# Optimization experiments

Hardware: AMD Instinct MI355X
Metric: run time of the kernel (lower is better)

The kernel has to match this reference:

```python
import jax, jax.numpy as jnp
import numpy as np

N_HEAD = 16

def setup_inputs() -> dict:
    key = jax.random.key(0)
    ks = jax.random.split(key, 5)
    B, T, C = 2, 2048, 1024
    s = 1.0 / np.sqrt(C)
    return {
        "x":  jax.random.normal(ks[0], (B, T, C), jnp.float32),
        "Wk": jax.random.normal(ks[1], (C, C), jnp.float32) * s,
        "Wq": jax.random.normal(ks[2], (C, C), jnp.float32) * s,
        "Wv": jax.random.normal(ks[3], (C, C), jnp.float32) * s,
        "Wp": jax.random.normal(ks[4], (C, C), jnp.float32) * s,
    }

def reference(x, Wk, Wq, Wv, Wp):
    B, T, C = x.shape
    H = N_HEAD
    D = C // H
    # torch Linear (bias=False): y = x @ W.T
    def proj(W):
        return (x @ W.T).reshape(B, T, H, D).transpose(0, 2, 1, 3)  # [B,H,T,D]
    q, k, v = proj(Wq), proj(Wk), proj(Wv)
    att = jnp.einsum("bhtd,bhsd->bhts", q, k) / jnp.sqrt(jnp.float32(D))
    causal = jnp.tril(jnp.ones((T, T), dtype=bool))
    att = jnp.where(causal[None, None], att, -jnp.inf)
    att = jax.nn.softmax(att, axis=-1)
    y = jnp.einsum("bhts,bhsd->bhtd", att, v)
    y = y.transpose(0, 2, 1, 3).reshape(B, T, C)
    return y @ Wp.T
```

## Files before the change

### kernel.cpp

```cpp
#include <hip/hip_runtime.h>

typedef unsigned short u16;
typedef unsigned int u32;
typedef unsigned long long u64;
typedef __attribute__((ext_vector_type(8))) short bf16x8;
typedef __attribute__((ext_vector_type(4))) float f32x4;

#define GLOAD16(gp, lp) __builtin_amdgcn_global_load_lds( \
  (const __attribute__((address_space(1))) unsigned int*)(gp), \
  (__attribute__((address_space(3))) unsigned int*)(lp), 16, 0, 0)

__device__ __forceinline__ u16 f2bf(float f) {
  unsigned int u = __builtin_bit_cast(unsigned int, f);
  u += 0x7fffu + ((u >> 16) & 1u);
  return (u16)(u >> 16);
}

__device__ __forceinline__ u32 pk2(float a, float b) {
  return (u32)f2bf(a) | ((u32)f2bf(b) << 16);
}

__global__ __launch_bounds__(256) void cvt_f32_bf16(
    const float* __restrict__ in, u16* __restrict__ out, int n) {
  int i = (blockIdx.x * 256 + threadIdx.x) * 4;
  if (i < n) {
    float4 f = *reinterpret_cast<const float4*>(in + i);
    u64 v = (u64)pk2(f.x, f.y) | ((u64)pk2(f.z, f.w) << 32);
    *reinterpret_cast<u64*>(out + i) = v;
  }
}

__global__ __launch_bounds__(256) void cvt_w4(
    const float* __restrict__ w0, const float* __restrict__ w1,
    const float* __restrict__ w2, const float* __restrict__ w3,
    u16* __restrict__ o0, u16* __restrict__ o1,
    u16* __restrict__ o2, u16* __restrict__ o3) {
  int z = blockIdx.y;
  const float* in = (z == 0) ? w0 : (z == 1) ? w1 : (z == 2) ? w2 : w3;
  u16* out = (z == 0) ? o0 : (z == 1) ? o1 : (z == 2) ? o2 : o3;
  int i = (blockIdx.x * 256 + threadIdx.x) * 4;
  float4 f = *reinterpret_cast<const float4*>(in + i);
  u64 v = (u64)pk2(f.x, f.y) | ((u64)pk2(f.z, f.w) << 32);
  *reinterpret_cast<u64*>(out + i) = v;
}

template<int MODE>
__device__ __forceinline__ void gemm_bt_body(
    const u16* __restrict__ A, const u16* __restrict__ Bw, void* __restrict__ Cout,
    int m0, int n0, float scale) {
  const int K = 1024;
  __shared__ __align__(16) u16 As[2][128 * 32];
  __shared__ __align__(16) u16 Bs[2][128 * 32];
  const int tid = threadIdx.x;
  const int lane = tid & 63, wid = tid >> 6;
  const int wr = wid >> 1, wc = wid & 1;
  const int g = lane >> 4, c = lane & 15;
  f32x4 acc[4][4] = {};

  auto stage = [&](int buf, int k0) {
#pragma unroll
    for (int i = 0; i < 2; ++i) {
      int idx = tid + i * 256;
      int row = idx >> 2, slot = idx & 3;
      int ss = slot ^ (row & 3);
      GLOAD16(A + (size_t)(m0 + row) * K + k0 + ss * 8, &As[buf][idx * 8]);
    }
#pragma unroll
    for (int i = 0; i < 2; ++i) {
      int idx = tid + i * 256;
      int row = idx >> 2, slot = idx & 3;
      int ss = slot ^ (row & 3);
      GLOAD16(Bw + (size_t)(n0 + row) * K + k0 + ss * 8, &Bs[buf][idx * 8]);
    }
  };

  stage(0, 0);
  __syncthreads();
  int buf = 0;
  for (int kt = 0; kt < 32; ++kt) {
    if (kt + 1 < 32) stage(buf ^ 1, (kt + 1) * 32);
    bf16x8 af[4], bfr[4];
#pragma unroll
    for (int mi = 0; mi < 4; ++mi) {
      int row = wr * 64 + mi * 16 + c;
      int slot = g ^ (row & 3);
      af[mi] = *(const bf16x8*)&As[buf][row * 32 + slot * 8];
    }
#pragma unroll
    for (int ni = 0; ni < 4; ++ni) {
      int row = wc * 64 + ni * 16 + c;
      int slot = g ^ (row & 3);
      bfr[ni] = *(const bf16x8*)&Bs[buf][row * 32 + slot * 8];
    }
    __builtin_amdgcn_s_setprio(1);
#pragma unroll
    for (int mi = 0; mi < 4; ++mi)
#pragma unroll
      for (int ni = 0; ni < 4; ++ni)
        acc[mi][ni] = __builtin_amdgcn_mfma_f32_16x16x32_bf16(af[mi], bfr[ni], acc[mi][ni], 0, 0, 0);
    __builtin_amdgcn_s_setprio(0);
    __syncthreads();
    buf ^= 1;
  }

#pragma unroll
  for (int mi = 0; mi < 4; ++mi)
#pragma unroll
    for (int ni = 0; ni < 4; ++ni)
#pragma unroll
      for (int i = 0; i < 4; ++i) {
        int m = m0 + wr * 64 + mi * 16 + g * 4 + i;
        int n = n0 + wc * 64 + ni * 16 + c;
        float v = acc[mi][ni][i];
        if (MODE == 0) {
          int b = m >> 11, t = m & 2047, h = n >> 6, d = n & 63;
          ((u16*)Cout)[(((size_t)b * 16 + h) * 2048 + t) * 64 + d] = f2bf(v * scale);
        } else {
          ((float*)Cout)[(size_t)m * 1024 + n] = v;
        }
      }
}

#define QSCALE 0.1803368801111204f

__global__ __launch_bounds__(256, 2) void proj_qkv(
    const u16* __restrict__ xb, const u16* __restrict__ wq, const u16* __restrict__ wk,
    const u16* __restrict__ wv, u16* __restrict__ q, u16* __restrict__ k, u16* __restrict__ v) {
  int z = blockIdx.z;
  const u16* W = (z == 0) ? wq : (z == 1) ? wk : wv;
  u16* O = (z == 0) ? q : (z == 1) ? k : v;
  float scale = (z == 0) ? QSCALE : 1.0f;
  gemm_bt_body<0>(xb, W, O, blockIdx.y * 128, blockIdx.x * 128, scale);
}

__global__ __launch_bounds__(256, 2) void gemm_out(
    const u16* __restrict__ y, const u16* __restrict__ wp, float* __restrict__ out) {
  gemm_bt_body<1>(y, wp, out, blockIdx.y * 128, blockIdx.x * 128, 1.0f);
}

__global__ __launch_bounds__(256) void transpose_v_kernel(
    const u16* __restrict__ v, u16* __restrict__ vt) {
  __shared__ u16 tile[64][65];
  int bh = blockIdx.y, t0 = blockIdx.x * 64;
  const u16* src = v + ((size_t)bh * 2048 + t0) * 64;
  u16* dst = vt + (size_t)bh * 64 * 2048 + t0;
  int tid = threadIdx.x;
#pragma unroll
  for (int i = 0; i < 16; ++i) {
    int idx = tid + i * 256;
    tile[idx >> 6][idx & 63] = src[idx];
  }
  __syncthreads();
#pragma unroll
  for (int i = 0; i < 16; ++i) {
    int idx = tid + i * 256;
    int d = idx >> 6, j = idx & 63;
    int t = ((j & 3) << 4) | (j >> 2);
    dst[(size_t)d * 2048 + j] = tile[t][d];
  }
}

__global__ __launch_bounds__(256, 2) void attn_kernel(
    const u16* __restrict__ q, const u16* __restrict__ kg,
    const u16* __restrict__ vt, u16* __restrict__ y) {
  const int T = 2048;
  __shared__ __align__(16) u16 Ks[2][128 * 64];
  __shared__ __align__(16) u16 Vs[2][64 * 128];
  __shared__ __align__(16) u16 Ps[4][16 * 128];
  const int tid = threadIdx.x, lane = tid & 63, w = tid >> 6;
  const int g = lane >> 4, c = lane & 15;
  const int bh = blockIdx.x;
  const u16* Q = q + (size_t)bh * T * 64;
  const u16* K = kg + (size_t)bh * T * 64;
  const u16* V = vt + (size_t)bh * 64 * T;
  const int b = bh >> 4, h = bh & 15;

  bf16x8 ones;
#pragma unroll
  for (int j = 0; j < 8; ++j) ones[j] = (short)0x3F80;

  auto stage = [&](int bb, int j0) {
#pragma unroll
    for (int i = 0; i < 4; ++i) {
      int idx = tid + i * 256;
      int row = idx >> 3, slot = idx & 7;
      int ss = slot ^ (row & 7);
      GLOAD16(K + (size_t)(j0 + row) * 64 + ss * 8, &Ks[bb][idx * 8]);
    }
#pragma unroll
    for (int i = 0; i < 4; ++i) {
      int idx = tid + i * 256;
      int d = idx >> 4, sub = (idx >> 3) & 1, s8 = idx & 7;
      int ss = s8 ^ (d & 7);
      GLOAD16(V + (size_t)d * T + j0 + sub * 64 + ss * 8, &Vs[bb][idx * 8]);
    }
  };

#pragma unroll 1
  for (int pass = 0; pass < 2; ++pass) {
    const int qt = pass ? (31 - (int)blockIdx.y) : (int)blockIdx.y;
    const int qrow0 = qt * 64 + w * 16;

    bf16x8 qf[2];
#pragma unroll
    for (int kk = 0; kk < 2; ++kk)
      qf[kk] = *(const bf16x8*)&Q[(size_t)(qrow0 + c) * 64 + kk * 32 + g * 8];

    f32x4 o[4] = {};
    f32x4 ol = {};

    const int nkt = (qt + 2) >> 1;
    stage(0, 0);
    __syncthreads();
    int buf = 0;
#pragma unroll 1
    for (int kt = 0; kt < nkt; ++kt) {
      const int j0 = kt * 128;
      if (kt + 1 < nkt) stage(buf ^ 1, j0 + 128);

      f32x4 s[8];
#pragma unroll
      for (int sub = 0; sub < 2; ++sub) {
        bf16x8 kb[4][2];
#pragma unroll
        for (int ni = 0; ni < 4; ++ni)
#pragma unroll
          for (int kk = 0; kk < 2; ++kk) {
            int kr = sub * 64 + ni * 16 + c;
            int slot = (kk * 4 + g) ^ (kr & 7);
            kb[ni][kk] = *(const bf16x8*)&Ks[buf][kr * 64 + slot * 8];
          }
        __builtin_amdgcn_s_setprio(1);
#pragma unroll
        for (int ni = 0; ni < 4; ++ni) {
          f32x4 a = {0.f, 0.f, 0.f, 0.f};
          a = __builtin_amdgcn_mfma_f32_16x16x32_bf16(qf[0], kb[ni][0], a, 0, 0, 0);
          a = __builtin_amdgcn_mfma_f32_16x16x32_bf16(qf[1], kb[ni][1], a, 0, 0, 0);
          s[sub * 4 + ni] = a;
        }
        __builtin_amdgcn_s_setprio(0);
      }

      const bool dumask = (kt == nkt - 1);
#pragma unroll
      for (int ni = 0; ni < 8; ++ni)
#pragma unroll
        for (int i = 0; i < 4; ++i) {
          float val = s[ni][i];
          if (dumask) {
            int row = qrow0 + g * 4 + i;
            int col = j0 + ni * 16 + c;
            if (col > row) val = -3.0e38f;
          }
          s[ni][i] = __builtin_amdgcn_exp2f(val);
        }

#pragma unroll
      for (int i = 0; i < 4; ++i) {
        int r = g * 4 + i;
        int slot = (c >> 1) ^ (r & 7);
#pragma unroll
        for (int sub = 0; sub < 2; ++sub) {
          u64 val = (u64)pk2(s[sub * 4 + 0][i], s[sub * 4 + 1][i]) |
                    ((u64)pk2(s[sub * 4 + 2][i], s[sub * 4 + 3][i]) << 32);
          *(u64*)((char*)&Ps[w][0] + r * 256 + sub * 128 + slot * 16 + (c & 1) * 8) = val;
        }
      }

      bf16x8 pa[2][2], vb[4][2][2];
#pragma unroll
      for (int sub = 0; sub < 2; ++sub)
#pragma unroll
        for (int kk = 0; kk < 2; ++kk) {
          int slot = (kk * 4 + g) ^ (c & 7);
          pa[sub][kk] = *(const bf16x8*)&Ps[w][c * 128 + sub * 64 + slot * 8];
        }
#pragma unroll
      for (int di = 0; di < 4; ++di)
#pragma unroll
        for (int sub = 0; sub < 2; ++sub)
#pragma unroll
          for (int kk = 0; kk < 2; ++kk) {
            int d = di * 16 + c;
            int slot = (kk * 4 + g) ^ (d & 7);
            vb[di][sub][kk] = *(const bf16x8*)&Vs[buf][d * 128 + sub * 64 + slot * 8];
          }
      __builtin_amdgcn_s_setprio(1);
#pragma unroll
      for (int sub = 0; sub < 2; ++sub) {
        ol = __builtin_amdgcn_mfma_f32_16x16x32_bf16(pa[sub][0], ones, ol, 0, 0, 0);
        ol = __builtin_amdgcn_mfma_f32_16x16x32_bf16(pa[sub][1], ones, ol, 0, 0, 0);
      }
#pragma unroll
      for (int di = 0; di < 4; ++di)
#pragma unroll
        for (int sub = 0; sub < 2; ++sub) {
          o[di] = __builtin_amdgcn_mfma_f32_16x16x32_bf16(pa[sub][0], vb[di][sub][0], o[di], 0, 0, 0);
          o[di] = __builtin_amdgcn_mfma_f32_16x16x32_bf16(pa[sub][1], vb[di][sub][1], o[di], 0, 0, 0);
        }
      __builtin_amdgcn_s_setprio(0);
      __syncthreads();
      buf ^= 1;
    }

#pragma unroll
    for (int i = 0; i < 4; ++i) {
      float inv = 1.f / ol[i];
      int t = qrow0 + g * 4 + i;
#pragma unroll
      for (int di = 0; di < 4; ++di) {
        int col = h * 64 + di * 16 + c;
        y[((size_t)b * 2048 + t) * 1024 + col] = f2bf(o[di][i] * inv);
      }
    }
  }
}

extern "C" void kernel_launch(void* const* d_in, const int* in_sizes, int n_in,
                              void* d_out, int out_size, void* d_ws, size_t ws_size,
                              hipStream_t stream) {
  const float* x  = (const float*)d_in[0];
  const float* Wk = (const float*)d_in[1];
  const float* Wq = (const float*)d_in[2];
  const float* Wv = (const float*)d_in[3];
  const float* Wp = (const float*)d_in[4];
  float* out = (float*)d_out;

  char* ws = (char*)d_ws;
  const size_t SZ_X = (size_t)4096 * 1024 * 2;
  const size_t SZ_W = (size_t)1024 * 1024 * 2;
  u16* xb  = (u16*)(ws);
  u16* qb  = (u16*)(ws + SZ_X);
  u16* kb  = (u16*)(ws + 2 * SZ_X);
  u16* vb  = (u16*)(ws + 3 * SZ_X);
  u16* wqb = (u16*)(ws + 4 * SZ_X);
  u16* wkb = (u16*)(ws + 4 * SZ_X + SZ_W);
  u16* wvb = (u16*)(ws + 4 * SZ_X + 2 * SZ_W);
  u16* wpb = (u16*)(ws + 4 * SZ_X + 3 * SZ_W);

  cvt_f32_bf16<<<4096, 256, 0, stream>>>(x, xb, 4096 * 1024);
  cvt_w4<<<dim3(1024, 4), 256, 0, stream>>>(Wq, Wk, Wv, Wp, wqb, wkb, wvb, wpb);

  proj_qkv<<<dim3(8, 32, 3), 256, 0, stream>>>(xb, wqb, wkb, wvb, qb, kb, vb);

  u16* vtb = xb;
  transpose_v_kernel<<<dim3(32, 32), 256, 0, stream>>>(vb, vtb);

  u16* yb = vb;
  attn_kernel<<<dim3(32, 16), 256, 0, stream>>>(qb, kb, vtb, yb);

  gemm_out<<<dim3(8, 32), 256, 0, stream>>>(yb, wpb, out);
}
```

Before: 120.1 us.

## Split attention into one q-tile per block with 64-wide KV tiles; halve out-GEMM M tile

The attention kernel now gives each block a single 64-row query tile, heaviest first, instead of pairing two tiles per block. It also shrinks the KV tile from 128 to 64 keys, which cuts LDS use and allows higher occupancy. The grid doubles to 1024 blocks. The output GEMM uses 64-row M tiles so it launches twice as many blocks, and the launch-bounds hints are raised. The trade-offs are more loop iterations and barriers per KV token, possibly worse load balance without the pairing, and less reuse per block in the out-projection.

```diff
diff --git a/kernel.cpp b/kernel.cpp
--- a/kernel.cpp
+++ b/kernel.cpp
@@ -44,22 +44,22 @@
   *reinterpret_cast<u64*>(out + i) = v;
 }
 
-template<int MODE>
+template<int MODE, int MI>
 __device__ __forceinline__ void gemm_bt_body(
     const u16* __restrict__ A, const u16* __restrict__ Bw, void* __restrict__ Cout,
     int m0, int n0, float scale) {
   const int K = 1024;
-  __shared__ __align__(16) u16 As[2][128 * 32];
+  __shared__ __align__(16) u16 As[2][MI * 32 * 32];
   __shared__ __align__(16) u16 Bs[2][128 * 32];
   const int tid = threadIdx.x;
   const int lane = tid & 63, wid = tid >> 6;
   const int wr = wid >> 1, wc = wid & 1;
   const int g = lane >> 4, c = lane & 15;
-  f32x4 acc[4][4] = {};
+  f32x4 acc[MI][4] = {};
 
   auto stage = [&](int buf, int k0) {
 #pragma unroll
-    for (int i = 0; i < 2; ++i) {
+    for (int i = 0; i < MI / 2; ++i) {
       int idx = tid + i * 256;
       int row = idx >> 2, slot = idx & 3;
       int ss = slot ^ (row & 3);
@@ -79,10 +79,10 @@
   int buf = 0;
   for (int kt = 0; kt < 32; ++kt) {
     if (kt + 1 < 32) stage(buf ^ 1, (kt + 1) * 32);
-    bf16x8 af[4], bfr[4];
-#pragma unroll
-    for (int mi = 0; mi < 4; ++mi) {
-      int row = wr * 64 + mi * 16 + c;
+    bf16x8 af[MI], bfr[4];
+#pragma unroll
+    for (int mi = 0; mi < MI; ++mi) {
+      int row = wr * (MI * 16) + mi * 16 + c;
       int slot = g ^ (row & 3);
       af[mi] = *(const bf16x8*)&As[buf][row * 32 + slot * 8];
     }
@@ -94,7 +94,7 @@
     }
     __builtin_amdgcn_s_setprio(1);
 #pragma unroll
-    for (int mi = 0; mi < 4; ++mi)
+    for (int mi = 0; mi < MI; ++mi)
 #pragma unroll
       for (int ni = 0; ni < 4; ++ni)
         acc[mi][ni] = __builtin_amdgcn_mfma_f32_16x16x32_bf16(af[mi], bfr[ni], acc[mi][ni], 0, 0, 0);
@@ -104,12 +104,12 @@
   }
 
 #pragma unroll
-  for (int mi = 0; mi < 4; ++mi)
+  for (int mi = 0; mi < MI; ++mi)
 #pragma unroll
     for (int ni = 0; ni < 4; ++ni)
 #pragma unroll
       for (int i = 0; i < 4; ++i) {
-        int m = m0 + wr * 64 + mi * 16 + g * 4 + i;
+        int m = m0 + wr * (MI * 16) + mi * 16 + g * 4 + i;
         int n = n0 + wc * 64 + ni * 16 + c;
         float v = acc[mi][ni][i];
         if (MODE == 0) {
@@ -123,19 +123,19 @@
 
 #define QSCALE 0.1803368801111204f
 
-__global__ __launch_bounds__(256, 2) void proj_qkv(
+__global__ __launch_bounds__(256, 3) void proj_qkv(
     const u16* __restrict__ xb, const u16* __restrict__ wq, const u16* __restrict__ wk,
     const u16* __restrict__ wv, u16* __restrict__ q, u16* __restrict__ k, u16* __restrict__ v) {
   int z = blockIdx.z;
   const u16* W = (z == 0) ? wq : (z == 1) ? wk : wv;
   u16* O = (z == 0) ? q : (z == 1) ? k : v;
   float scale = (z == 0) ? QSCALE : 1.0f;
-  gemm_bt_body<0>(xb, W, O, blockIdx.y * 128, blockIdx.x * 128, scale);
+  gemm_bt_body<0, 4>(xb, W, O, blockIdx.y * 128, blockIdx.x * 128, scale);
 }
 
 __global__ __launch_bounds__(256, 2) void gemm_out(
     const u16* __restrict__ y, const u16* __restrict__ wp, float* __restrict__ out) {
-  gemm_bt_body<1>(y, wp, out, blockIdx.y * 128, blockIdx.x * 128, 1.0f);
+  gemm_bt_body<1, 2>(y, wp, out, blockIdx.y * 64, blockIdx.x * 128, 1.0f);
 }
 
 __global__ __launch_bounds__(256) void transpose_v_kernel(
@@ -160,20 +160,22 @@
   }
 }
 
-__global__ __launch_bounds__(256, 2) void attn_kernel(
+__global__ __launch_bounds__(256, 4) void attn_kernel(
     const u16* __restrict__ q, const u16* __restrict__ kg,
     const u16* __restrict__ vt, u16* __restrict__ y) {
   const int T = 2048;
-  __shared__ __align__(16) u16 Ks[2][128 * 64];
-  __shared__ __align__(16) u16 Vs[2][64 * 128];
-  __shared__ __align__(16) u16 Ps[4][16 * 128];
+  __shared__ __align__(16) u16 Ks[2][64 * 64];
+  __shared__ __align__(16) u16 Vs[2][64 * 64];
+  __shared__ __align__(16) u16 Ps[4][16 * 64];
   const int tid = threadIdx.x, lane = tid & 63, w = tid >> 6;
   const int g = lane >> 4, c = lane & 15;
   const int bh = blockIdx.x;
+  const int qt = 31 - (int)blockIdx.y;
   const u16* Q = q + (size_t)bh * T * 64;
   const u16* K = kg + (size_t)bh * T * 64;
   const u16* V = vt + (size_t)bh * 64 * T;
   const int b = bh >> 4, h = bh & 15;
+  const int qrow0 = qt * 64 + w * 16;
 
   bf16x8 ones;
 #pragma unroll
@@ -181,137 +183,109 @@
 
   auto stage = [&](int bb, int j0) {
 #pragma unroll
-    for (int i = 0; i < 4; ++i) {
+    for (int i = 0; i < 2; ++i) {
       int idx = tid + i * 256;
       int row = idx >> 3, slot = idx & 7;
       int ss = slot ^ (row & 7);
       GLOAD16(K + (size_t)(j0 + row) * 64 + ss * 8, &Ks[bb][idx * 8]);
-    }
+      GLOAD16(V + (size_t)row * T + j0 + ss * 8, &Vs[bb][idx * 8]);
+    }
+  };
+
+  bf16x8 qf[2];
+#pragma unroll
+  for (int kk = 0; kk < 2; ++kk)
+    qf[kk] = *(const bf16x8*)&Q[(size_t)(qrow0 + c) * 64 + kk * 32 + g * 8];
+
+  f32x4 o[4] = {};
+  f32x4 ol = {};
+
+  const int nkt = qt + 1;
+  stage(0, 0);
+  __syncthreads();
+  int buf = 0;
+#pragma unroll 1
+  for (int kt = 0; kt < nkt; ++kt) {
+    const int j0 = kt * 64;
+    if (kt + 1 < nkt) stage(buf ^ 1, j0 + 64);
+
+    bf16x8 kb[4][2];
+#pragma unroll
+    for (int ni = 0; ni < 4; ++ni)
+#pragma unroll
+      for (int kk = 0; kk < 2; ++kk) {
+        int kr = ni * 16 + c;
+        int slot = (kk * 4 + g) ^ (kr & 7);
+        kb[ni][kk] = *(const bf16x8*)&Ks[buf][kr * 64 + slot * 8];
+      }
+    f32x4 s[4];
+    __builtin_amdgcn_s_setprio(1);
+#pragma unroll
+    for (int ni = 0; ni < 4; ++ni) {
+      f32x4 a = {0.f, 0.f, 0.f, 0.f};
+      a = __builtin_amdgcn_mfma_f32_16x16x32_bf16(qf[0], kb[ni][0], a, 0, 0, 0);
+      a = __builtin_amdgcn_mfma_f32_16x16x32_bf16(qf[1], kb[ni][1], a, 0, 0, 0);
+      s[ni] = a;
+    }
+    __builtin_amdgcn_s_setprio(0);
+
+    const bool dumask = (kt == qt);
+#pragma unroll
+    for (int ni = 0; ni < 4; ++ni)
+#pragma unroll
+      for (int i = 0; i < 4; ++i) {
+        float val = s[ni][i];
+        if (dumask) {
+          int row = qrow0 + g * 4 + i;
+          int col = j0 + ni * 16 + c;
+          if (col > row) val = -3.0e38f;
+        }
+        s[ni][i] = __builtin_amdgcn_exp2f(val);
+      }
+
 #pragma unroll
     for (int i = 0; i < 4; ++i) {
-      int idx = tid + i * 256;
-      int d = idx >> 4, sub = (idx >> 3) & 1, s8 = idx & 7;
-      int ss = s8 ^ (d & 7);
-      GLOAD16(V + (size_t)d * T + j0 + sub * 64 + ss * 8, &Vs[bb][idx * 8]);
-    }
-  };
-
-#pragma unroll 1
-  for (int pass = 0; pass < 2; ++pass) {
-    const int qt = pass ? (31 - (int)blockIdx.y) : (int)blockIdx.y;
-    const int qrow0 = qt * 64 + w * 16;
-
-    bf16x8 qf[2];
-#pragma unroll
-    for (int kk = 0; kk < 2; ++kk)
-      qf[kk] = *(const bf16x8*)&Q[(size_t)(qrow0 + c) * 64 + kk * 32 + g * 8];
-
-    f32x4 o[4] = {};
-    f32x4 ol = {};
-
-    const int nkt = (qt + 2) >> 1;
-    stage(0, 0);
+      int r = g * 4 + i;
+      int slot = (c >> 1) ^ (r & 7);
+      u64 val = (u64)pk2(s[0][i], s[1][i]) | ((u64)pk2(s[2][i], s[3][i]) << 32);
+      *(u64*)((char*)&Ps[w][0] + r * 128 + slot * 16 + (c & 1) * 8) = val;
+    }
+
+    bf16x8 pa[2], vb[4][2];
+#pragma unroll
+    for (int kk = 0; kk < 2; ++kk) {
+      int slot = (kk * 4 + g) ^ (c & 7);
+      pa[kk] = *(const bf16x8*)&Ps[w][c * 64 + slot * 8];
+    }
+#pragma unroll
+    for (int di = 0; di < 4; ++di)
+#pragma unroll
+      for (int kk = 0; kk < 2; ++kk) {
+        int d = di * 16 + c;
+        int slot = (kk * 4 + g) ^ (d & 7);
+        vb[di][kk] = *(const bf16x8*)&Vs[buf][d * 64 + slot * 8];
+      }
+    __builtin_amdgcn_s_setprio(1);
+    ol = __builtin_amdgcn_mfma_f32_16x16x32_bf16(pa[0], ones, ol, 0, 0, 0);
+    ol = __builtin_amdgcn_mfma_f32_16x16x32_bf16(pa[1], ones, ol, 0, 0, 0);
+#pragma unroll
+    for (int di = 0; di < 4; ++di) {
+      o[di] = __builtin_amdgcn_mfma_f32_16x16x32_bf16(pa[0], vb[di][0], o[di], 0, 0, 0);
+      o[di] = __builtin_amdgcn_mfma_f32_16x16x32_bf16(pa[1], vb[di][1], o[di], 0, 0, 0);
+    }
+    __builtin_amdgcn_s_setprio(0);
     __syncthreads();
-    int buf = 0;
-#pragma unroll 1
-    for (int kt = 0; kt < nkt; ++kt) {
-      const int j0 = kt * 128;
-      if (kt + 1 < nkt) stage(buf ^ 1, j0 + 128);
-
-      f32x4 s[8];
-#pragma unroll
-      for (int sub = 0; sub < 2; ++sub) {
-        bf16x8 kb[4][2];
-#pragma unroll
-        for (int ni = 0; ni < 4; ++ni)
-#pragma unroll
-          for (int kk = 0; kk < 2; ++kk) {
-            int kr = sub * 64 + ni * 16 + c;
-            int slot = (kk * 4 + g) ^ (kr & 7);
-            kb[ni][kk] = *(const bf16x8*)&Ks[buf][kr * 64 + slot * 8];
-          }
-        __builtin_amdgcn_s_setprio(1);
-#pragma unroll
-        for (int ni = 0; ni < 4; ++ni) {
-          f32x4 a = {0.f, 0.f, 0.f, 0.f};
-          a = __builtin_amdgcn_mfma_f32_16x16x32_bf16(qf[0], kb[ni][0], a, 0, 0, 0);
-          a = __builtin_amdgcn_mfma_f32_16x16x32_bf16(qf[1], kb[ni][1], a, 0, 0, 0);
-          s[sub * 4 + ni] = a;
-        }
-        __builtin_amdgcn_s_setprio(0);
-      }
-
-      const bool dumask = (kt == nkt - 1);
-#pragma unroll
-      for (int ni = 0; ni < 8; ++ni)
-#pragma unroll
-        for (int i = 0; i < 4; ++i) {
-          float val = s[ni][i];
-          if (dumask) {
-            int row = qrow0 + g * 4 + i;
-            int col = j0 + ni * 16 + c;
-            if (col > row) val = -3.0e38f;
-          }
-          s[ni][i] = __builtin_amdgcn_exp2f(val);
-        }
-
-#pragma unroll
-      for (int i = 0; i < 4; ++i) {
-        int r = g * 4 + i;
-        int slot = (c >> 1) ^ (r & 7);
-#pragma unroll
-        for (int sub = 0; sub < 2; ++sub) {
-          u64 val = (u64)pk2(s[sub * 4 + 0][i], s[sub * 4 + 1][i]) |
-                    ((u64)pk2(s[sub * 4 + 2][i], s[sub * 4 + 3][i]) << 32);
-          *(u64*)((char*)&Ps[w][0] + r * 256 + sub * 128 + slot * 16 + (c & 1) * 8) = val;
-        }
-      }
-
-      bf16x8 pa[2][2], vb[4][2][2];
-#pragma unroll
-      for (int sub = 0; sub < 2; ++sub)
-#pragma unroll
-        for (int kk = 0; kk < 2; ++kk) {
-          int slot = (kk * 4 + g) ^ (c & 7);
-          pa[sub][kk] = *(const bf16x8*)&Ps[w][c * 128 + sub * 64 + slot * 8];
-        }
-#pragma unroll
-      for (int di = 0; di < 4; ++di)
-#pragma unroll
-        for (int sub = 0; sub < 2; ++sub)
-#pragma unroll
-          for (int kk = 0; kk < 2; ++kk) {
-            int d = di * 16 + c;
-            int slot = (kk * 4 + g) ^ (d & 7);
-            vb[di][sub][kk] = *(const bf16x8*)&Vs[buf][d * 128 + sub * 64 + slot * 8];
-          }
-      __builtin_amdgcn_s_setprio(1);
-#pragma unroll
-      for (int sub = 0; sub < 2; ++sub) {
-        ol = __builtin_amdgcn_mfma_f32_16x16x32_bf16(pa[sub][0], ones, ol, 0, 0, 0);
-        ol = __builtin_amdgcn_mfma_f32_16x16x32_bf16(pa[sub][1], ones, ol, 0, 0, 0);
-      }
-#pragma unroll
-      for (int di = 0; di < 4; ++di)
-#pragma unroll
-        for (int sub = 0; sub < 2; ++sub) {
-          o[di] = __builtin_amdgcn_mfma_f32_16x16x32_bf16(pa[sub][0], vb[di][sub][0], o[di], 0, 0, 0);
-          o[di] = __builtin_amdgcn_mfma_f32_16x16x32_bf16(pa[sub][1], vb[di][sub][1], o[di], 0, 0, 0);
-        }
-      __builtin_amdgcn_s_setprio(0);
-      __syncthreads();
-      buf ^= 1;
-    }
-
-#pragma unroll
-    for (int i = 0; i < 4; ++i) {
-      float inv = 1.f / ol[i];
-      int t = qrow0 + g * 4 + i;
-#pragma unroll
-      for (int di = 0; di < 4; ++di) {
-        int col = h * 64 + di * 16 + c;
-        y[((size_t)b * 2048 + t) * 1024 + col] = f2bf(o[di][i] * inv);
-      }
+    buf ^= 1;
+  }
+
+#pragma unroll
+  for (int i = 0; i < 4; ++i) {
+    float inv = 1.f / ol[i];
+    int t = qrow0 + g * 4 + i;
+#pragma unroll
+    for (int di = 0; di < 4; ++di) {
+      int col = h * 64 + di * 16 + c;
+      y[((size_t)b * 2048 + t) * 1024 + col] = f2bf(o[di][i] * inv);
     }
   }
 }
@@ -347,7 +321,7 @@
   transpose_v_kernel<<<dim3(32, 32), 256, 0, stream>>>(vb, vtb);
 
   u16* yb = vb;
-  attn_kernel<<<dim3(32, 16), 256, 0, stream>>>(qb, kb, vtb, yb);
-
-  gemm_out<<<dim3(8, 32), 256, 0, stream>>>(yb, wpb, out);
-}
+  attn_kernel<<<dim3(32, 32), 256, 0, stream>>>(qb, kb, vtb, yb);
+
+  gemm_out<<<dim3(8, 64), 256, 0, stream>>>(yb, wpb, out);
+}
```

Result: faster. 114.6 us (-4.5%).
